# Performance work log

Measured on AMD Instinct MI355X. Metric: run time of the kernel, lower is better.

The kernel has to match this reference:

```python
import jax, jax.numpy as jnp
import numpy as np


def _conv1x1(x, w, b):
    # x: (b, c_in, t, h, w); w: (c_out, c_in); b: (c_out,)
    return jnp.einsum('bcthw,oc->bothw', x, w) + b[None, :, None, None, None]


def _maxpool_hw(x):
    # MaxPool3d(kernel=(1,2,2)): pool spatial dims by 2 (h, w assumed even)
    b, c, t, h, w = x.shape
    return x.reshape(b, c, t, h // 2, 2, w // 2, 2).max(axis=(4, 6))


def setup_inputs() -> dict:
    key = jax.random.key(0)
    ks = jax.random.split(key, 9)
    C, CI = 256, 128  # in_channels, inter_channels = in_channels // 2
    B, T, H, W = 8, 8, 28, 28
    s = 1.0 / np.sqrt(C)
    si = 1.0 / np.sqrt(CI)
    return {
        'x': jax.random.normal(ks[0], (B, C, T, H, W), jnp.float32),
        'g_w': jax.random.normal(ks[1], (CI, C), jnp.float32) * s,
        'g_b': jax.random.normal(ks[2], (CI,), jnp.float32) * 0.01,
        'theta_w': jax.random.normal(ks[3], (CI, C), jnp.float32) * s,
        'theta_b': jax.random.normal(ks[4], (CI,), jnp.float32) * 0.01,
        'phi_w': jax.random.normal(ks[5], (CI, C), jnp.float32) * s,
        'phi_b': jax.random.normal(ks[6], (CI,), jnp.float32) * 0.01,
        'W_w': jax.random.normal(ks[7], (C, CI), jnp.float32) * si,
        'W_b': jax.random.normal(ks[8], (C,), jnp.float32) * 0.01,
    }


def reference(x, g_w, g_b, theta_w, theta_b, phi_w, phi_b, W_w, W_b):
    b, c, t, h, w = x.shape
    ci = g_w.shape[0]
    # g and phi paths are sub-sampled by MaxPool3d(1,2,2)
    g_x = _maxpool_hw(_conv1x1(x, g_w, g_b)).reshape(b, ci, -1)          # (b, ci, M)
    g_x = g_x.transpose(0, 2, 1)                                          # (b, M, ci)
    theta_x = _conv1x1(x, theta_w, theta_b).reshape(b, ci, -1)            # (b, ci, N)
    theta_x = theta_x.transpose(0, 2, 1)                                  # (b, N, ci)
    phi_x = _maxpool_hw(_conv1x1(x, phi_w, phi_b)).reshape(b, ci, -1)     # (b, ci, M)
    f = jnp.einsum('bnc,bcm->bnm', theta_x, phi_x)                        # (b, N, M)
    f_div_C = jax.nn.softmax(f, axis=-1)
    y = jnp.einsum('bnm,bmc->bnc', f_div_C, g_x)                          # (b, N, ci)
    y = y.transpose(0, 2, 1).reshape(b, ci, t, h, w)
    W_y = _conv1x1(y, W_w, W_b)
    return W_y + x
```

## Files before the change

### kernel.cpp

```cpp
#include <hip/hip_runtime.h>

typedef _Float16 f16;
typedef f16 half8 __attribute__((ext_vector_type(8)));
typedef float f32x4 __attribute__((ext_vector_type(4)));

#define MFMA16(a, b, c) __builtin_amdgcn_mfma_f32_16x16x32_f16((a), (b), (c), 0, 0, 0)

static constexpr int B = 8, C = 256, CI = 128, N = 6272, M = 1568, MP = 1600;

static constexpr size_t oXT = 0;
static constexpr size_t oQ  = (size_t)B * N * C;
static constexpr size_t oPF = oQ  + (size_t)B * N * CI;
static constexpr size_t oGF = oPF + (size_t)B * N * CI;
static constexpr size_t oPP = oGF + (size_t)B * N * CI;
static constexpr size_t oGT = oPP + (size_t)B * MP * CI;
static constexpr size_t oW  = oGT + (size_t)B * MP * CI;

static __device__ __forceinline__ half8 hmax8(half8 a, half8 b) {
    half8 r;
#pragma unroll
    for (int j = 0; j < 8; j++) r[j] = a[j] > b[j] ? a[j] : b[j];
    return r;
}

static __device__ __forceinline__ float rowmax16(float x) {
    int t;
    t = __builtin_amdgcn_update_dpp(__float_as_int(x), __float_as_int(x), 0x121, 0xF, 0xF, false);
    x = fmaxf(x, __int_as_float(t));
    t = __builtin_amdgcn_update_dpp(__float_as_int(x), __float_as_int(x), 0x122, 0xF, 0xF, false);
    x = fmaxf(x, __int_as_float(t));
    t = __builtin_amdgcn_update_dpp(__float_as_int(x), __float_as_int(x), 0x124, 0xF, 0xF, false);
    x = fmaxf(x, __int_as_float(t));
    t = __builtin_amdgcn_update_dpp(__float_as_int(x), __float_as_int(x), 0x128, 0xF, 0xF, false);
    x = fmaxf(x, __int_as_float(t));
    return x;
}

__global__ void k_prep(const float* tw, const float* pw, const float* gw,
                       const float* Ww, f16* dst) {
    int i = blockIdx.x * 256 + threadIdx.x;
    int s = i >> 15, j = i & 32767;
    float v;
    if (s == 0) v = tw[j];
    else if (s == 1) v = pw[j];
    else if (s == 2) v = gw[j];
    else v = Ww[j];
    dst[i] = (f16)v;
}

__global__ void k_trans(const float* x, f16* xT) {
    __shared__ float tile[32][33];
    int b = blockIdx.z, nt = blockIdx.x, ct = blockIdx.y;
    int tx = threadIdx.x, ty = threadIdx.y;
#pragma unroll
    for (int i = 0; i < 4; i++) {
        int c = ct * 32 + ty + i * 8;
        tile[ty + i * 8][tx] = x[(size_t)(b * C + c) * N + nt * 32 + tx];
    }
    __syncthreads();
#pragma unroll
    for (int i = 0; i < 4; i++) {
        int n = nt * 32 + ty + i * 8;
        xT[(size_t)(b * N + n) * C + ct * 32 + tx] = (f16)tile[tx][ty + i * 8];
    }
}

__global__ __launch_bounds__(256) void k_proj(const f16* __restrict__ xT,
                                              const f16* __restrict__ w16,
                                              const float* __restrict__ bias,
                                              f16* __restrict__ out) {
    __shared__ f16 xs[128 * 72];
    __shared__ f16 ws[128 * 72];
    int b = blockIdx.z, n0 = blockIdx.x * 128;
    int tid = threadIdx.x, w = tid >> 6, lane = tid & 63, ln = lane & 15, quad = lane >> 4;
    f32x4 acc[2][8];
#pragma unroll
    for (int rb = 0; rb < 2; rb++)
#pragma unroll
        for (int cb = 0; cb < 8; cb++) acc[rb][cb] = (f32x4){0.f, 0.f, 0.f, 0.f};

    for (int kc = 0; kc < 4; kc++) {
#pragma unroll
        for (int i = 0; i < 4; i++) {
            int qq = tid + i * 256;
            int row = qq >> 3, coff = (qq & 7) * 8;
            *(int4*)&xs[row * 72 + coff] =
                *(const int4*)&xT[(size_t)(b * N + n0 + row) * C + kc * 64 + coff];
            *(int4*)&ws[row * 72 + coff] =
                *(const int4*)&w16[(size_t)row * C + kc * 64 + coff];
        }
        __syncthreads();
#pragma unroll
        for (int ks = 0; ks < 2; ks++) {
            half8 a0 = *(const half8*)&xs[(w * 32 + ln) * 72 + ks * 32 + quad * 8];
            half8 a1 = *(const half8*)&xs[(w * 32 + 16 + ln) * 72 + ks * 32 + quad * 8];
#pragma unroll
            for (int cb = 0; cb < 8; cb++) {
                half8 bf = *(const half8*)&ws[(cb * 16 + ln) * 72 + ks * 32 + quad * 8];
                acc[0][cb] = MFMA16(a0, bf, acc[0][cb]);
                acc[1][cb] = MFMA16(a1, bf, acc[1][cb]);
            }
        }
        __syncthreads();
    }
#pragma unroll
    for (int cb = 0; cb < 8; cb++) {
        float bv = bias[cb * 16 + ln];
#pragma unroll
        for (int rb = 0; rb < 2; rb++) {
#pragma unroll
            for (int r = 0; r < 4; r++) {
                int n = n0 + w * 32 + rb * 16 + quad * 4 + r;
                out[(size_t)(b * N + n) * CI + cb * 16 + ln] = (f16)(acc[rb][cb][r] + bv);
            }
        }
    }
}

__global__ __launch_bounds__(256) void k_pool(const f16* __restrict__ phiF, const f16* __restrict__ gF,
                                              f16* __restrict__ phiP, f16* __restrict__ gPT) {
    __shared__ f16 gt[128 * 72];
    int b = blockIdx.y, mt = blockIdx.x;
    int tid = threadIdx.x;
#pragma unroll
    for (int i = 0; i < 4; i++) {
        int qq = tid + i * 256;
        int ml = qq >> 4, coff = (qq & 15) * 8;
        int m = mt * 64 + ml;
        half8 pv, gv;
        if (m < M) {
            int t = m / 196, rr = m % 196, hp = rr / 14, wp = rr % 14;
            int nb = t * 784 + hp * 56 + wp * 2;
            size_t base = ((size_t)(b * N) + nb) * CI + coff;
            half8 p0 = *(const half8*)&phiF[base];
            half8 p1 = *(const half8*)&phiF[base + CI];
            half8 p2 = *(const half8*)&phiF[base + 28 * CI];
            half8 p3 = *(const half8*)&phiF[base + 29 * CI];
            pv = hmax8(hmax8(p0, p1), hmax8(p2, p3));
            half8 g0 = *(const half8*)&gF[base];
            half8 g1 = *(const half8*)&gF[base + CI];
            half8 g2 = *(const half8*)&gF[base + 28 * CI];
            half8 g3 = *(const half8*)&gF[base + 29 * CI];
            gv = hmax8(hmax8(g0, g1), hmax8(g2, g3));
        } else {
#pragma unroll
            for (int j = 0; j < 8; j++) { pv[j] = (f16)0.f; gv[j] = (f16)0.f; }
        }
        *(half8*)&phiP[((size_t)b * MP + m) * CI + coff] = pv;
#pragma unroll
        for (int j = 0; j < 8; j++) gt[(coff + j) * 72 + ml] = gv[j];
    }
    __syncthreads();
#pragma unroll
    for (int i = 0; i < 4; i++) {
        int qq = tid + i * 256;
        int ci = qq >> 3, moff = (qq & 7) * 8;
        *(int4*)&gPT[((size_t)(b * CI) + ci) * MP + mt * 64 + moff] = *(const int4*)&gt[ci * 72 + moff];
    }
}

__global__ __launch_bounds__(256, 2) void k_attn(const f16* __restrict__ q,
                                                 const f16* __restrict__ kk,
                                                 const f16* __restrict__ v,
                                                 f16* __restrict__ y) {
    __shared__ f16 Ks[64 * 136];
    __shared__ f16 Vs[128 * 72];
    __shared__ f16 Ps[4 * 32 * 72];
    int b = blockIdx.y, n0 = blockIdx.x * 128;
    int tid = threadIdx.x, w = tid >> 6, lane = tid & 63, ln = lane & 15, quad = lane >> 4;
    int wq = n0 + w * 32;
    f16* Pw = &Ps[w * 32 * 72];

    half8 qf[2][4];
#pragma unroll
    for (int qt = 0; qt < 2; qt++)
#pragma unroll
        for (int ks = 0; ks < 4; ks++) {
            qf[qt][ks] = *(const half8*)&q[(size_t)(b * N + wq + qt * 16 + ln) * CI + ks * 32 + quad * 8];
#pragma unroll
            for (int j = 0; j < 8; j++) qf[qt][ks][j] *= (f16)1.4426950408889634f;
        }

    f32x4 O[2][8], Osum[2];
#pragma unroll
    for (int qt = 0; qt < 2; qt++) {
        Osum[qt] = (f32x4){0.f, 0.f, 0.f, 0.f};
#pragma unroll
        for (int cb = 0; cb < 8; cb++) O[qt][cb] = (f32x4){0.f, 0.f, 0.f, 0.f};
    }
    float mi[2][4] = {{-1e30f, -1e30f, -1e30f, -1e30f}, {-1e30f, -1e30f, -1e30f, -1e30f}};

    for (int mc = 0; mc < 25; mc++) {
#pragma unroll
        for (int i = 0; i < 4; i++) {
            int qq = tid + i * 256;
            int kr = qq >> 4, kc = (qq & 15) * 8;
            *(int4*)&Ks[kr * 136 + kc] = *(const int4*)&kk[((size_t)b * MP + mc * 64 + kr) * CI + kc];
            int vr = qq >> 3, vc = (qq & 7) * 8;
            *(int4*)&Vs[vr * 72 + vc] = *(const int4*)&v[((size_t)(b * CI) + vr) * MP + mc * 64 + vc];
        }
        __syncthreads();

        f32x4 S[2][4];
#pragma unroll
        for (int mt = 0; mt < 4; mt++) {
            f32x4 s0 = (f32x4){0.f, 0.f, 0.f, 0.f}, s1 = (f32x4){0.f, 0.f, 0.f, 0.f};
#pragma unroll
            for (int ks = 0; ks < 4; ks++) {
                half8 kb = *(const half8*)&Ks[(mt * 16 + ln) * 136 + ks * 32 + quad * 8];
                s0 = MFMA16(qf[0][ks], kb, s0);
                s1 = MFMA16(qf[1][ks], kb, s1);
            }
            S[0][mt] = s0; S[1][mt] = s1;
        }

#pragma unroll
        for (int qt = 0; qt < 2; qt++)
#pragma unroll
            for (int r = 0; r < 4; r++) {
                float vm = fmaxf(fmaxf(S[qt][0][r], S[qt][1][r]), fmaxf(S[qt][2][r], S[qt][3][r]));
                vm = rowmax16(vm);
                float mnew = fmaxf(mi[qt][r], vm);
                float alpha = __builtin_amdgcn_exp2f(mi[qt][r] - mnew);
                mi[qt][r] = mnew;
#pragma unroll
                for (int mt = 0; mt < 4; mt++) {
                    float p = __builtin_amdgcn_exp2f(S[qt][mt][r] - mnew);
                    Pw[(qt * 16 + quad * 4 + r) * 72 + mt * 16 + ln] = (f16)p;
                }
#pragma unroll
                for (int cb = 0; cb < 8; cb++) O[qt][cb][r] *= alpha;
                Osum[qt][r] *= alpha;
            }

#pragma unroll
        for (int ks = 0; ks < 2; ks++) {
            half8 a0 = *(const half8*)&Pw[ln * 72 + ks * 32 + quad * 8];
            half8 a1 = *(const half8*)&Pw[(16 + ln) * 72 + ks * 32 + quad * 8];
            f16 ov = (mc * 64 + ks * 32 < M) ? (f16)1.0f : (f16)0.0f;
            half8 on;
#pragma unroll
            for (int j = 0; j < 8; j++) on[j] = ov;
#pragma unroll
            for (int cb = 0; cb < 8; cb++) {
                half8 bv = *(const half8*)&Vs[(cb * 16 + ln) * 72 + ks * 32 + quad * 8];
                O[0][cb] = MFMA16(a0, bv, O[0][cb]);
                O[1][cb] = MFMA16(a1, bv, O[1][cb]);
            }
            Osum[0] = MFMA16(a0, on, Osum[0]);
            Osum[1] = MFMA16(a1, on, Osum[1]);
        }
        __syncthreads();
    }

#pragma unroll
    for (int qt = 0; qt < 2; qt++)
#pragma unroll
        for (int cb = 0; cb < 8; cb++)
#pragma unroll
            for (int r = 0; r < 4; r++) {
                int n = wq + qt * 16 + quad * 4 + r;
                y[(size_t)(b * N + n) * CI + cb * 16 + ln] = (f16)(O[qt][cb][r] / Osum[qt][r]);
            }
}

__global__ __launch_bounds__(256) void k_final(const f16* __restrict__ y,
                                               const f16* __restrict__ Ww,
                                               const float* __restrict__ Wb,
                                               const float* __restrict__ x,
                                               float* __restrict__ out) {
    __shared__ f16 ys[64 * 136];
    __shared__ f16 Ws[128 * 136];
    int b = blockIdx.z, ch = blockIdx.y, n0 = blockIdx.x * 64;
    int tid = threadIdx.x, w = tid >> 6, lane = tid & 63, ln = lane & 15, quad = lane >> 4;
#pragma unroll
    for (int i = 0; i < 4; i++) {
        int qq = tid + i * 256; int row = qq >> 4, coff = (qq & 15) * 8;
        *(int4*)&ys[row * 136 + coff] =
            *(const int4*)&y[(size_t)(b * N + n0 + row) * CI + coff];
    }
#pragma unroll
    for (int i = 0; i < 8; i++) {
        int qq = tid + i * 256; int row = qq >> 4, coff = (qq & 15) * 8;
        *(int4*)&Ws[row * 136 + coff] =
            *(const int4*)&Ww[(size_t)(ch * 128 + row) * CI + coff];
    }
    __syncthreads();
    f32x4 acc[2][4];
#pragma unroll
    for (int rb = 0; rb < 2; rb++)
#pragma unroll
        for (int nb = 0; nb < 4; nb++) acc[rb][nb] = (f32x4){0.f, 0.f, 0.f, 0.f};
#pragma unroll
    for (int ks = 0; ks < 4; ks++) {
        half8 a0 = *(const half8*)&Ws[(w * 32 + ln) * 136 + ks * 32 + quad * 8];
        half8 a1 = *(const half8*)&Ws[(w * 32 + 16 + ln) * 136 + ks * 32 + quad * 8];
#pragma unroll
        for (int nb = 0; nb < 4; nb++) {
            half8 bf = *(const half8*)&ys[(nb * 16 + ln) * 136 + ks * 32 + quad * 8];
            acc[0][nb] = MFMA16(a0, bf, acc[0][nb]);
            acc[1][nb] = MFMA16(a1, bf, acc[1][nb]);
        }
    }
#pragma unroll
    for (int rb = 0; rb < 2; rb++) {
        int cbase = ch * 128 + w * 32 + rb * 16 + quad * 4;
#pragma unroll
        for (int nb = 0; nb < 4; nb++) {
#pragma unroll
            for (int r = 0; r < 4; r++) {
                int c = cbase + r;
                size_t addr = (size_t)(b * C + c) * N + n0 + nb * 16 + ln;
                out[addr] = acc[rb][nb][r] + Wb[c] + x[addr];
            }
        }
    }
}

extern "C" void kernel_launch(void* const* d_in, const int* in_sizes, int n_in,
                              void* d_out, int out_size, void* d_ws, size_t ws_size,
                              hipStream_t stream) {
    const float* x  = (const float*)d_in[0];
    const float* gw = (const float*)d_in[1];
    const float* gb = (const float*)d_in[2];
    const float* tw = (const float*)d_in[3];
    const float* tb = (const float*)d_in[4];
    const float* pw = (const float*)d_in[5];
    const float* pb = (const float*)d_in[6];
    const float* Ww = (const float*)d_in[7];
    const float* Wb = (const float*)d_in[8];
    float* out = (float*)d_out;
    f16* ws = (f16*)d_ws;

    f16* xT   = ws + oXT;
    f16* Q    = ws + oQ;
    f16* phiF = ws + oPF;
    f16* gF   = ws + oGF;
    f16* phiP = ws + oPP;
    f16* gPT  = ws + oGT;
    f16* Y    = ws + oPF;
    f16* w16  = ws + oW;

    k_prep<<<512, 256, 0, stream>>>(tw, pw, gw, Ww, w16);
    k_trans<<<dim3(196, 8, 8), dim3(32, 8), 0, stream>>>(x, xT);
    k_proj<<<dim3(49, 1, 8), 256, 0, stream>>>(xT, w16,         tb, Q);
    k_proj<<<dim3(49, 1, 8), 256, 0, stream>>>(xT, w16 + 32768, pb, phiF);
    k_proj<<<dim3(49, 1, 8), 256, 0, stream>>>(xT, w16 + 65536, gb, gF);
    k_pool<<<dim3(25, 8), 256, 0, stream>>>(phiF, gF, phiP, gPT);
    k_attn<<<dim3(49, 8), 256, 0, stream>>>(Q, phiP, gPT, Y);
    k_final<<<dim3(98, 2, 8), 256, 0, stream>>>(Y, w16 + 98304, Wb, x, out);
    (void)in_sizes; (void)n_in; (void)out_size; (void)ws_size;
}
```

Measured before the change: 269.1 us.

## Fuse transpose and three projections into one kernel; halve attention block size

```diff
diff --git a/kernel.cpp b/kernel.cpp
--- a/kernel.cpp
+++ b/kernel.cpp
@@ -8,8 +8,7 @@
 
 static constexpr int B = 8, C = 256, CI = 128, N = 6272, M = 1568, MP = 1600;
 
-static constexpr size_t oXT = 0;
-static constexpr size_t oQ  = (size_t)B * N * C;
+static constexpr size_t oQ  = 0;
 static constexpr size_t oPF = oQ  + (size_t)B * N * CI;
 static constexpr size_t oGF = oPF + (size_t)B * N * CI;
 static constexpr size_t oPP = oGF + (size_t)B * N * CI;
@@ -48,70 +47,74 @@
     dst[i] = (f16)v;
 }
 
-__global__ void k_trans(const float* x, f16* xT) {
-    __shared__ float tile[32][33];
-    int b = blockIdx.z, nt = blockIdx.x, ct = blockIdx.y;
-    int tx = threadIdx.x, ty = threadIdx.y;
-#pragma unroll
-    for (int i = 0; i < 4; i++) {
-        int c = ct * 32 + ty + i * 8;
-        tile[ty + i * 8][tx] = x[(size_t)(b * C + c) * N + nt * 32 + tx];
-    }
-    __syncthreads();
-#pragma unroll
-    for (int i = 0; i < 4; i++) {
-        int n = nt * 32 + ty + i * 8;
-        xT[(size_t)(b * N + n) * C + ct * 32 + tx] = (f16)tile[tx][ty + i * 8];
-    }
-}
-
-__global__ __launch_bounds__(256) void k_proj(const f16* __restrict__ xT,
-                                              const f16* __restrict__ w16,
-                                              const float* __restrict__ bias,
-                                              f16* __restrict__ out) {
-    __shared__ f16 xs[128 * 72];
-    __shared__ f16 ws[128 * 72];
-    int b = blockIdx.z, n0 = blockIdx.x * 128;
+__global__ __launch_bounds__(256) void k_projf(const float* __restrict__ x,
+                                               const f16* __restrict__ w16,
+                                               const float* __restrict__ tb,
+                                               const float* __restrict__ pb,
+                                               const float* __restrict__ gb,
+                                               f16* __restrict__ Q,
+                                               f16* __restrict__ phiF,
+                                               f16* __restrict__ gF) {
+    __shared__ f16 xs[64 * 72];
+    __shared__ f16 ws[384 * 72];
+    int b = blockIdx.y, n0 = blockIdx.x * 64;
     int tid = threadIdx.x, w = tid >> 6, lane = tid & 63, ln = lane & 15, quad = lane >> 4;
-    f32x4 acc[2][8];
-#pragma unroll
-    for (int rb = 0; rb < 2; rb++)
-#pragma unroll
-        for (int cb = 0; cb < 8; cb++) acc[rb][cb] = (f32x4){0.f, 0.f, 0.f, 0.f};
+    int nl = tid & 63, cg = tid >> 6;
+
+    f32x4 acc[4][6];
+#pragma unroll
+    for (int nt = 0; nt < 4; nt++)
+#pragma unroll
+        for (int cb = 0; cb < 6; cb++) acc[nt][cb] = (f32x4){0.f, 0.f, 0.f, 0.f};
 
     for (int kc = 0; kc < 4; kc++) {
 #pragma unroll
-        for (int i = 0; i < 4; i++) {
+        for (int i = 0; i < 12; i++) {
             int qq = tid + i * 256;
             int row = qq >> 3, coff = (qq & 7) * 8;
-            *(int4*)&xs[row * 72 + coff] =
-                *(const int4*)&xT[(size_t)(b * N + n0 + row) * C + kc * 64 + coff];
             *(int4*)&ws[row * 72 + coff] =
                 *(const int4*)&w16[(size_t)row * C + kc * 64 + coff];
         }
+        {
+            half8 h0, h1;
+#pragma unroll
+            for (int j = 0; j < 8; j++)
+                h0[j] = (f16)x[(size_t)(b * C + kc * 64 + cg * 16 + j) * N + n0 + nl];
+#pragma unroll
+            for (int j = 0; j < 8; j++)
+                h1[j] = (f16)x[(size_t)(b * C + kc * 64 + cg * 16 + 8 + j) * N + n0 + nl];
+            *(half8*)&xs[nl * 72 + cg * 16] = h0;
+            *(half8*)&xs[nl * 72 + cg * 16 + 8] = h1;
+        }
         __syncthreads();
 #pragma unroll
         for (int ks = 0; ks < 2; ks++) {
-            half8 a0 = *(const half8*)&xs[(w * 32 + ln) * 72 + ks * 32 + quad * 8];
-            half8 a1 = *(const half8*)&xs[(w * 32 + 16 + ln) * 72 + ks * 32 + quad * 8];
-#pragma unroll
-            for (int cb = 0; cb < 8; cb++) {
-                half8 bf = *(const half8*)&ws[(cb * 16 + ln) * 72 + ks * 32 + quad * 8];
-                acc[0][cb] = MFMA16(a0, bf, acc[0][cb]);
-                acc[1][cb] = MFMA16(a1, bf, acc[1][cb]);
+            half8 af[4];
+#pragma unroll
+            for (int nt = 0; nt < 4; nt++)
+                af[nt] = *(const half8*)&xs[(nt * 16 + ln) * 72 + ks * 32 + quad * 8];
+#pragma unroll
+            for (int cb = 0; cb < 6; cb++) {
+                half8 bf = *(const half8*)&ws[(w * 96 + cb * 16 + ln) * 72 + ks * 32 + quad * 8];
+#pragma unroll
+                for (int nt = 0; nt < 4; nt++) acc[nt][cb] = MFMA16(af[nt], bf, acc[nt][cb]);
             }
         }
         __syncthreads();
     }
 #pragma unroll
-    for (int cb = 0; cb < 8; cb++) {
-        float bv = bias[cb * 16 + ln];
-#pragma unroll
-        for (int rb = 0; rb < 2; rb++) {
+    for (int cb = 0; cb < 6; cb++) {
+        int cig = w * 96 + cb * 16;
+        int sel = cig >> 7, cil = (cig & 127) + ln;
+        const float* bp = sel == 0 ? tb : (sel == 1 ? pb : gb);
+        f16* outp = sel == 0 ? Q : (sel == 1 ? phiF : gF);
+        float bv = bp[cil];
+#pragma unroll
+        for (int nt = 0; nt < 4; nt++) {
 #pragma unroll
             for (int r = 0; r < 4; r++) {
-                int n = n0 + w * 32 + rb * 16 + quad * 4 + r;
-                out[(size_t)(b * N + n) * CI + cb * 16 + ln] = (f16)(acc[rb][cb][r] + bv);
+                int n = n0 + nt * 16 + quad * 4 + r;
+                outp[(size_t)(b * N + n) * CI + cil] = (f16)(acc[nt][cb][r] + bv);
             }
         }
     }
@@ -159,14 +162,14 @@
     }
 }
 
-__global__ __launch_bounds__(256, 2) void k_attn(const f16* __restrict__ q,
+__global__ __launch_bounds__(128, 2) void k_attn(const f16* __restrict__ q,
                                                  const f16* __restrict__ kk,
                                                  const f16* __restrict__ v,
                                                  f16* __restrict__ y) {
     __shared__ f16 Ks[64 * 136];
     __shared__ f16 Vs[128 * 72];
-    __shared__ f16 Ps[4 * 32 * 72];
-    int b = blockIdx.y, n0 = blockIdx.x * 128;
+    __shared__ f16 Ps[2 * 32 * 72];
+    int b = blockIdx.y, n0 = blockIdx.x * 64;
     int tid = threadIdx.x, w = tid >> 6, lane = tid & 63, ln = lane & 15, quad = lane >> 4;
     int wq = n0 + w * 32;
     f16* Pw = &Ps[w * 32 * 72];
@@ -192,8 +195,8 @@
 
     for (int mc = 0; mc < 25; mc++) {
 #pragma unroll
-        for (int i = 0; i < 4; i++) {
-            int qq = tid + i * 256;
+        for (int i = 0; i < 8; i++) {
+            int qq = tid + i * 128;
             int kr = qq >> 4, kc = (qq & 15) * 8;
             *(int4*)&Ks[kr * 136 + kc] = *(const int4*)&kk[((size_t)b * MP + mc * 64 + kr) * CI + kc];
             int vr = qq >> 3, vc = (qq & 7) * 8;
@@ -332,7 +335,6 @@
     float* out = (float*)d_out;
     f16* ws = (f16*)d_ws;
 
-    f16* xT   = ws + oXT;
     f16* Q    = ws + oQ;
     f16* phiF = ws + oPF;
     f16* gF   = ws + oGF;
@@ -342,12 +344,9 @@
     f16* w16  = ws + oW;
 
     k_prep<<<512, 256, 0, stream>>>(tw, pw, gw, Ww, w16);
-    k_trans<<<dim3(196, 8, 8), dim3(32, 8), 0, stream>>>(x, xT);
-    k_proj<<<dim3(49, 1, 8), 256, 0, stream>>>(xT, w16,         tb, Q);
-    k_proj<<<dim3(49, 1, 8), 256, 0, stream>>>(xT, w16 + 32768, pb, phiF);
-    k_proj<<<dim3(49, 1, 8), 256, 0, stream>>>(xT, w16 + 65536, gb, gF);
+    k_projf<<<dim3(98, 8), 256, 0, stream>>>(x, w16, tb, pb, gb, Q, phiF, gF);
     k_pool<<<dim3(25, 8), 256, 0, stream>>>(phiF, gF, phiP, gPT);
-    k_attn<<<dim3(49, 8), 256, 0, stream>>>(Q, phiP, gPT, Y);
+    k_attn<<<dim3(98, 8), 128, 0, stream>>>(Q, phiP, gPT, Y);
     k_final<<<dim3(98, 2, 8), 256, 0, stream>>>(Y, w16 + 98304, Wb, x, out);
     (void)in_sizes; (void)n_in; (void)out_size; (void)ws_size;
 }
```

New measurement: 463.1 us. 72.1% more time.
